# Kernel optimization log

Hardware: AMD Instinct MI355X
Metric: run time of the kernel (lower is better)

The kernel has to match this reference:

```python
import jax, jax.numpy as jnp
import numpy as np


def _conv1x1(x, W, b):
    # x: (B, Ci, H, W), W: (Co, Ci), b: (Co,)
    return jnp.einsum('oi,bihw->bohw', W, x) + b[None, :, None, None]


def setup_inputs() -> dict:
    key = jax.random.key(0)
    ks = jax.random.split(key, 12)
    B, C, H, W = 4, 256, 64, 64
    d = C // 2
    prev_c = 512
    s = lambda k, shape, scale=0.05: (jax.random.normal(k, shape, dtype=jnp.float32) * scale)
    return {
        'source_enc_f': jax.random.normal(ks[0], (B, C, H, W), dtype=jnp.float32),
        'target_enc_f': jax.random.normal(ks[1], (B, C, H, W), dtype=jnp.float32),
        'prev_inp': jax.random.normal(ks[2], (B, prev_c, H // 2, W // 2), dtype=jnp.float32),
        'Wq': s(ks[3], (d, C)), 'bq': s(ks[4], (d,)),
        'Wk': s(ks[5], (d, C)), 'bk': s(ks[6], (d,)),
        'Wv': s(ks[7], (d, C)), 'bv': s(ks[8], (d,)),
        'Wp': s(ks[9], (C, d)), 'bp': s(ks[10], (C,)),
        'gamma': jnp.zeros((1,), dtype=jnp.float32) + 0.1,  # nonzero so attn path contributes
        'Wc': s(ks[11], (C, C + prev_c, 3, 3)),
        'bc': jnp.zeros((C,), dtype=jnp.float32),
    }


def reference(source_enc_f, target_enc_f, prev_inp, Wq, bq, Wk, bk, Wv, bv, Wp, bp, gamma, Wc, bc):
    B, C, H, W = source_enc_f.shape
    d = Wq.shape[0]
    HW = H * W

    # --- AttnMech ---
    q = _conv1x1(source_enc_f, Wq, bq)   # (B, d, H, W)
    k = _conv1x1(target_enc_f, Wk, bk)
    v = _conv1x1(target_enc_f, Wv, bv)

    kf = k.reshape(B, d, HW)             # (B, d, HW)
    qf = q.reshape(B, d, HW)             # (B, d, HW)
    # scores[b, i, j] = sum_c key[b, c, i] * query[b, c, j]; no 1/sqrt(d) scaling
    scores = jnp.einsum('bci,bcj->bij', kf, qf)       # (B, HW, HW)
    attn = jax.nn.softmax(scores, axis=1)             # softmax over key axis (torch dim=1)

    vf = v.transpose(0, 2, 3, 1).reshape(B, HW, d)    # (B, HW, d)
    out = jnp.einsum('bij,bjc->bic', attn, vf)        # (B, HW, d)
    out = out.reshape(B, H, W, d).transpose(0, 3, 1, 2)  # (B, d, H, W)
    out = _conv1x1(out, Wp, bp)                       # (B, C, H, W)
    x = target_enc_f + gamma[0] * out

    # --- upsample (nearest, scale 2) + concat ---
    prev = jnp.repeat(jnp.repeat(prev_inp, 2, axis=2), 2, axis=3)
    x = jnp.concatenate([x, prev], axis=1)            # (B, C+prev_c, H, W)

    # --- 3x3 conv, stride 1, pad 1 ---
    x = jax.lax.conv_general_dilated(
        x, Wc, window_strides=(1, 1), padding=((1, 1), (1, 1)),
        dimension_numbers=('NCHW', 'OIHW', 'NCHW'))
    x = x + bc[None, :, None, None]

    # --- InstanceNorm2d (affine=False, eps=1e-5, biased var over HW) ---
    mean = jnp.mean(x, axis=(2, 3), keepdims=True)
    var = jnp.mean(jnp.square(x - mean), axis=(2, 3), keepdims=True)
    x = (x - mean) * jax.lax.rsqrt(var + 1e-5)

    return jax.nn.relu(x)
```

## Files before the change

### kernel.cpp

```cpp
#include <hip/hip_runtime.h>
#include <hip/hip_bf16.h>

#define BB 4
#define CC 256
#define HW 4096
#define DD 128

typedef __attribute__((ext_vector_type(8))) short bf16x8;
typedef __attribute__((ext_vector_type(4))) short bf16x4;
typedef __attribute__((ext_vector_type(4))) float f32x4;

static __device__ __forceinline__ void ld4(float* dst, const float* src) {
  float4 t = *(const float4*)src;
  dst[0] = t.x; dst[1] = t.y; dst[2] = t.z; dst[3] = t.w;
}

static __device__ __forceinline__ short f2b(float f) {
  unsigned u = __float_as_uint(f);
  u += 0x7fffu + ((u >> 16) & 1u);
  return (short)(u >> 16);
}
static __device__ __forceinline__ unsigned pk2(float lo, float hi) {
  return (unsigned)(unsigned short)f2b(lo) | ((unsigned)(unsigned short)f2b(hi) << 16);
}

static __device__ __forceinline__ void gl16(const short* g, short* l) {
  __builtin_amdgcn_global_load_lds(
      (const __attribute__((address_space(1))) unsigned*)g,
      (__attribute__((address_space(3))) unsigned*)l, 16, 0, 0);
}

__global__ __launch_bounds__(256) void k_qkv_mfma(
    const float* __restrict__ src, const float* __restrict__ tgt,
    const float* __restrict__ Wq, const float* __restrict__ bq,
    const float* __restrict__ Wk, const float* __restrict__ bk,
    const float* __restrict__ Wv, const float* __restrict__ bv,
    short* __restrict__ qb, short* __restrict__ kb, short* __restrict__ vb)
{
  __shared__ __align__(16) short Wt[128 * 40];
  __shared__ __align__(16) short Xt[64 * 40];
  __shared__ __align__(16) short T[9216];
  const int tid = threadIdx.x;
  const int wv = tid >> 6;
  const int lane = tid & 63;
  const int t = lane & 15, q = lane >> 4;
  const int px0 = blockIdx.x * 64;
  const int which = blockIdx.y;
  const int b = blockIdx.z;
  const float* X    = (which == 0) ? src : tgt;
  const float* Wm   = (which == 0) ? Wq : (which == 1) ? Wk : Wv;
  const float* bias = (which == 0) ? bq : (which == 1) ? bk : bv;

  const f32x4 zf = {0.f, 0.f, 0.f, 0.f};
  f32x4 acc[2][4];
#pragma unroll
  for (int mt = 0; mt < 2; ++mt)
#pragma unroll
    for (int nt = 0; nt < 4; ++nt) acc[mt][nt] = zf;

  for (int kk = 0; kk < CC; kk += 32) {
    __syncthreads();
#pragma unroll
    for (int u = 0; u < 4; ++u) {
      int e = tid + (u << 8);
      int row = e >> 3, cq = (e & 7) * 4;
      float4 w4 = *(const float4*)&Wm[row * CC + kk + cq];
      unsigned* dst = (unsigned*)(Wt + row * 40 + cq);
      dst[0] = pk2(w4.x, w4.y);
      dst[1] = pk2(w4.z, w4.w);
    }
#pragma unroll
    for (int u = 0; u < 2; ++u) {
      int e = tid + (u << 8);
      int c = e >> 4, p4 = (e & 15) * 4;
      float4 xv = *(const float4*)&X[((size_t)b * CC + kk + c) * HW + px0 + p4];
      Xt[(p4 + 0) * 40 + c] = f2b(xv.x);
      Xt[(p4 + 1) * 40 + c] = f2b(xv.y);
      Xt[(p4 + 2) * 40 + c] = f2b(xv.z);
      Xt[(p4 + 3) * 40 + c] = f2b(xv.w);
    }
    __syncthreads();
    bf16x8 af[2], bfr[4];
#pragma unroll
    for (int mt = 0; mt < 2; ++mt)
      af[mt] = *(const bf16x8*)(Wt + (wv * 32 + mt * 16 + t) * 40 + q * 8);
#pragma unroll
    for (int nt = 0; nt < 4; ++nt)
      bfr[nt] = *(const bf16x8*)(Xt + (nt * 16 + t) * 40 + q * 8);
#pragma unroll
    for (int mt = 0; mt < 2; ++mt)
#pragma unroll
      for (int nt = 0; nt < 4; ++nt)
        acc[mt][nt] = __builtin_amdgcn_mfma_f32_16x16x32_bf16(
            af[mt], bfr[nt], acc[mt][nt], 0, 0, 0);
  }
  __syncthreads();
  if (which < 2) {
#pragma unroll
    for (int mt = 0; mt < 2; ++mt) {
      int chb = wv * 32 + mt * 16 + q * 4;
#pragma unroll
      for (int r = 0; r < 4; ++r) {
        float bv_ = bias[chb + r];
#pragma unroll
        for (int nt = 0; nt < 4; ++nt)
          T[(nt * 16 + t) * 136 + chb + r] = f2b(acc[mt][nt][r] + bv_);
      }
    }
    __syncthreads();
    short* out = (which == 0) ? qb : kb;
    int p = tid >> 2, cq = (tid & 3) * 32;
    short* gdst = out + ((size_t)b * HW + px0 + p) * DD + cq;
#pragma unroll
    for (int e2 = 0; e2 < 4; ++e2)
      *(uint4*)(gdst + e2 * 8) = *(const uint4*)(T + p * 136 + cq + e2 * 8);
  } else {
#pragma unroll
    for (int mt = 0; mt < 2; ++mt) {
      int chb = wv * 32 + mt * 16 + q * 4;
#pragma unroll
      for (int r = 0; r < 4; ++r) {
        float bv_ = bias[chb + r];
#pragma unroll
        for (int nt = 0; nt < 4; ++nt)
          T[(chb + r) * 72 + nt * 16 + t] = f2b(acc[mt][nt][r] + bv_);
      }
    }
    __syncthreads();
    int ch = tid >> 1, pq = (tid & 1) * 32;
    short* gdst = vb + ((size_t)b * DD + ch) * HW + px0 + pq;
#pragma unroll
    for (int e2 = 0; e2 < 4; ++e2)
      *(uint4*)(gdst + e2 * 8) = *(const uint4*)(T + ch * 72 + pq + e2 * 8);
  }
}

__global__ __launch_bounds__(256) void k_lsum2(
    const short* __restrict__ qb, const short* __restrict__ kb,
    float* __restrict__ rl)
{
  __shared__ float lred[4][64];
  const int tid = threadIdx.x;
  const int w = tid >> 6;
  const int lane = tid & 63;
  const int t = lane & 15, q = lane >> 4;
  const int j0 = blockIdx.x * 64;
  const int ibeg = blockIdx.y * 1024;
  const int b = blockIdx.z;
  const short* qbb = qb + (size_t)b * HW * DD;
  const short* kbb = kb + (size_t)b * HW * DD;

  bf16x8 Bq[4][4];
#pragma unroll
  for (int nt = 0; nt < 4; ++nt)
#pragma unroll
    for (int kk = 0; kk < 4; ++kk)
      Bq[nt][kk] = *(const bf16x8*)(qbb + (size_t)(j0 + nt * 16 + t) * DD + kk * 32 + q * 8);

  float racc[4] = {0.f, 0.f, 0.f, 0.f};
  const f32x4 zf = {0.f, 0.f, 0.f, 0.f};

  for (int i = ibeg + w * 16; i < ibeg + 1024; i += 64) {
    bf16x8 Ak[4];
#pragma unroll
    for (int kk = 0; kk < 4; ++kk)
      Ak[kk] = *(const bf16x8*)(kbb + (size_t)(i + t) * DD + kk * 32 + q * 8);
#pragma unroll
    for (int nt = 0; nt < 4; ++nt) {
      f32x4 d = zf;
#pragma unroll
      for (int kk = 0; kk < 4; ++kk)
        d = __builtin_amdgcn_mfma_f32_16x16x32_bf16(Ak[kk], Bq[nt][kk], d, 0, 0, 0);
      racc[nt] += __expf(d[0]) + __expf(d[1]) + __expf(d[2]) + __expf(d[3]);
    }
  }
#pragma unroll
  for (int nt = 0; nt < 4; ++nt) {
    float r = racc[nt];
    r += __shfl_xor(r, 16);
    r += __shfl_xor(r, 32);
    if (q == 0) lred[w][nt * 16 + t] = r;
  }
  __syncthreads();
  if (tid < 64) {
    float sum = lred[0][tid] + lred[1][tid] + lred[2][tid] + lred[3][tid];
    atomicAdd(&rl[(size_t)b * HW + j0 + tid], sum);
  }
}

__global__ __launch_bounds__(256) void k_vs(
    const short* __restrict__ vb, const float* __restrict__ rl,
    short* __restrict__ vs)
{
  int id4 = (blockIdx.x * 256 + threadIdx.x) * 4;
  int j = id4 & (HW - 1);
  int b = id4 >> 19;
  uint2 pv = *(const uint2*)(vb + id4);
  float f0 = __uint_as_float(pv.x << 16);
  float f1 = __uint_as_float(pv.x & 0xffff0000u);
  float f2 = __uint_as_float(pv.y << 16);
  float f3 = __uint_as_float(pv.y & 0xffff0000u);
  const float* rlb = rl + (size_t)b * HW + j;
  unsigned u0 = pk2(f0 / rlb[0], f1 / rlb[1]);
  unsigned u1 = pk2(f2 / rlb[2], f3 / rlb[3]);
  *(uint2*)(vs + id4) = make_uint2(u0, u1);
}

__global__ __launch_bounds__(256, 2) void k_attn2(
    const short* __restrict__ qb, const short* __restrict__ kb,
    const short* __restrict__ vs, float* __restrict__ ao)
{
  __shared__ __align__(16) short Qs[64 * 136];
  __shared__ __align__(16) short Vss[128 * 72];
  __shared__ __align__(16) short P[4][16][76];
  const int tid = threadIdx.x;
  const int w = tid >> 6;
  const int lane = tid & 63;
  const int t = lane & 15, q = lane >> 4;
  const int b = blockIdx.z;
  const int i0 = blockIdx.x * 64 + w * 16;
  const int jbeg = blockIdx.y * 2048, jend = jbeg + 2048;
  const short* qbb = qb + (size_t)b * HW * DD;
  const short* kbb = kb + (size_t)b * HW * DD;
  const short* vsb = vs + (size_t)b * DD * HW;
  const f32x4 zf = {0.f, 0.f, 0.f, 0.f};

  bf16x8 Ak[4];
#pragma unroll
  for (int kk = 0; kk < 4; ++kk)
    Ak[kk] = *(const bf16x8*)(kbb + (size_t)(i0 + t) * DD + kk * 32 + q * 8);

  f32x4 acc[8];
#pragma unroll
  for (int nt = 0; nt < 8; ++nt) acc[nt] = zf;

  bf16x8 rq[4], rv[4];
#pragma unroll
  for (int r = 0; r < 4; ++r) {
    int e = tid + (r << 8);
    rq[r] = *(const bf16x8*)(qbb + (size_t)(jbeg + (e >> 4)) * DD + (e & 15) * 8);
    rv[r] = *(const bf16x8*)(vsb + (size_t)(e >> 3) * HW + jbeg + (e & 7) * 8);
  }

  for (int j = jbeg; j < jend; j += 64) {
    __syncthreads();
#pragma unroll
    for (int r = 0; r < 4; ++r) {
      int e = tid + (r << 8);
      *(bf16x8*)(Qs + (e >> 4) * 136 + (e & 15) * 8) = rq[r];
      *(bf16x8*)(Vss + (e >> 3) * 72 + (e & 7) * 8) = rv[r];
    }
    __syncthreads();
    if (j + 64 < jend) {
#pragma unroll
      for (int r = 0; r < 4; ++r) {
        int e = tid + (r << 8);
        rq[r] = *(const bf16x8*)(qbb + (size_t)(j + 64 + (e >> 4)) * DD + (e & 15) * 8);
        rv[r] = *(const bf16x8*)(vsb + (size_t)(e >> 3) * HW + j + 64 + (e & 7) * 8);
      }
    }
    f32x4 sv[4];
#pragma unroll
    for (int nt = 0; nt < 4; ++nt) sv[nt] = zf;
#pragma unroll
    for (int nt = 0; nt < 4; ++nt)
#pragma unroll
      for (int kk = 0; kk < 4; ++kk) {
        bf16x8 bq = *(const bf16x8*)(Qs + (nt * 16 + t) * 136 + kk * 32 + q * 8);
        sv[nt] = __builtin_amdgcn_mfma_f32_16x16x32_bf16(Ak[kk], bq, sv[nt], 0, 0, 0);
      }
#pragma unroll
    for (int nt = 0; nt < 4; ++nt)
#pragma unroll
      for (int r = 0; r < 4; ++r)
        P[w][q * 4 + r][nt * 16 + t] = f2b(__expf(sv[nt][r]));
    bf16x8 ap[2];
#pragma unroll
    for (int ks = 0; ks < 2; ++ks) {
      bf16x4 lo = *(const bf16x4*)&P[w][t][ks * 32 + q * 8];
      bf16x4 hi = *(const bf16x4*)&P[w][t][ks * 32 + q * 8 + 4];
      ap[ks] = __builtin_shufflevector(lo, hi, 0, 1, 2, 3, 4, 5, 6, 7);
    }
#pragma unroll
    for (int nt = 0; nt < 8; ++nt)
#pragma unroll
      for (int ks = 0; ks < 2; ++ks) {
        bf16x8 bv = *(const bf16x8*)(Vss + (nt * 16 + t) * 72 + ks * 32 + q * 8);
        acc[nt] = __builtin_amdgcn_mfma_f32_16x16x32_bf16(ap[ks], bv, acc[nt], 0, 0, 0);
      }
  }
  float* aob = ao + (size_t)b * DD * HW;
#pragma unroll
  for (int nt = 0; nt < 8; ++nt)
#pragma unroll
    for (int r = 0; r < 4; ++r)
      atomicAdd(&aob[(size_t)(nt * 16 + t) * HW + i0 + q * 4 + r], acc[nt][r]);
}

__global__ __launch_bounds__(256) void k_proj(
    const float* __restrict__ ao, const float* __restrict__ tgt,
    const float* __restrict__ Wp, const float* __restrict__ bp,
    const float* __restrict__ gamma, short* __restrict__ Xn)
{
  __shared__ float Wt[32][132];
  __shared__ float Xs[32][68];
  __shared__ float T[64][133];
  const int tid = threadIdx.x;
  const int tx = tid & 15, ty = tid >> 4;
  const int p0 = blockIdx.x * 64;
  const int ro = blockIdx.y * 128;
  const int b = blockIdx.z;
  const float g0 = gamma[0];

  float acc[8][4];
#pragma unroll
  for (int i = 0; i < 8; ++i)
#pragma unroll
    for (int j = 0; j < 4; ++j) acc[i][j] = 0.f;

  for (int kk = 0; kk < DD; kk += 32) {
    __syncthreads();
#pragma unroll
    for (int u = 0; u < 4; ++u) {
      int e = tid + 256 * u;
      int c4 = (e & 7) * 4, r = e >> 3;
      float w[4]; ld4(w, &Wp[(ro + r) * DD + kk + c4]);
      Wt[c4 + 0][r] = w[0]; Wt[c4 + 1][r] = w[1];
      Wt[c4 + 2][r] = w[2]; Wt[c4 + 3][r] = w[3];
    }
#pragma unroll
    for (int u = 0; u < 2; ++u) {
      int e = tid + 256 * u;
      int p4 = (e & 15) * 4, c = e >> 4;
      *(float4*)&Xs[c][p4] = *(const float4*)&ao[(b * DD + kk + c) * HW + p0 + p4];
    }
    __syncthreads();
#pragma unroll 4
    for (int c = 0; c < 32; ++c) {
      float wa[8], xb[4];
      ld4(wa, &Wt[c][ty * 8]); ld4(wa + 4, &Wt[c][ty * 8 + 4]);
      ld4(xb, &Xs[c][tx * 4]);
#pragma unroll
      for (int rr = 0; rr < 8; ++rr)
#pragma unroll
        for (int pp = 0; pp < 4; ++pp) acc[rr][pp] += wa[rr] * xb[pp];
    }
  }
#pragma unroll
  for (int rr = 0; rr < 8; ++rr) {
    int r = ro + ty * 8 + rr;
    int idx = (b * CC + r) * HW + p0 + tx * 4;
    float4 t4 = *(const float4*)&tgt[idx];
    float bpv = bp[r];
    T[tx * 4 + 0][ty * 8 + rr] = t4.x + g0 * (acc[rr][0] + bpv);
    T[tx * 4 + 1][ty * 8 + rr] = t4.y + g0 * (acc[rr][1] + bpv);
    T[tx * 4 + 2][ty * 8 + rr] = t4.z + g0 * (acc[rr][2] + bpv);
    T[tx * 4 + 3][ty * 8 + rr] = t4.w + g0 * (acc[rr][3] + bpv);
  }
  __syncthreads();
  {
    int p = tid >> 2, cq = (tid & 3) * 32;
    int h = p0 >> 6;
    unsigned* dst = (unsigned*)(Xn + ((((size_t)b * 66 + h + 1) * 66) + 1 + p) * 768 + ro + cq);
#pragma unroll
    for (int e = 0; e < 16; ++e)
      dst[e] = pk2(T[p][cq + 2 * e], T[p][cq + 2 * e + 1]);
  }
}

__global__ __launch_bounds__(256) void k_pack(
    const float* __restrict__ prev, short* __restrict__ Xn)
{
  __shared__ float tile[64][65];
  const int tid = threadIdx.x;
  const int h = blockIdx.x;
  const int ci0 = blockIdx.y * 64;
  const int b = blockIdx.z;

  {
    int w = tid & 63, r = tid >> 6;
    for (int cs = r; cs < 64; cs += 4)
      tile[cs][w] = prev[((size_t)b * 512 + ci0 + cs) * 1024 + (h >> 1) * 32 + (w >> 1)];
  }
  __syncthreads();
  {
    int ci = tid & 63, wq = tid >> 6;
    for (int ws2 = wq; ws2 < 64; ws2 += 4)
      Xn[((((size_t)b * 66 + h + 1) * 66) + 1 + ws2) * 768 + 256 + ci0 + ci] = f2b(tile[ci][ws2]);
  }
}

__global__ __launch_bounds__(256) void k_wb(
    const float* __restrict__ Wc, short* __restrict__ Wb)
{
  int i = blockIdx.x * 256 + threadIdx.x;
  int o = i / 6912;
  int rem = i - o * 6912;
  int khw = rem / 768;
  int ci = rem - khw * 768;
  Wb[i] = f2b(Wc[(size_t)o * 6912 + ci * 9 + khw]);
}

__global__ __launch_bounds__(256, 2) void k_conv_mfma(
    const short* __restrict__ Xn,
    const short* __restrict__ Wb,
    const float* __restrict__ bcw,
    short* __restrict__ cb)
{
  __shared__ __align__(16) short Wl[384 * 64];
  __shared__ __align__(16) short Xl[66 * 64];
  const int tid = threadIdx.x;
  const int wv = tid >> 6;
  const int lane = tid & 63;
  const int t = lane & 15, q = lane >> 4;
  const int h = blockIdx.x;
  const int m0blk = blockIdx.y * 128;
  const int b = blockIdx.z;

  const f32x4 zf = {0.f, 0.f, 0.f, 0.f};
  f32x4 acc[2][4];
#pragma unroll
  for (int mt = 0; mt < 2; ++mt)
#pragma unroll
    for (int nt = 0; nt < 4; ++nt) acc[mt][nt] = zf;

  for (int kh = 0; kh < 3; ++kh) {
    const short* wsrc = Wb + (size_t)m0blk * 6912 + (kh * 3) * 768;
    const short* xsrc = Xn + ((size_t)b * 66 + h + kh) * 66 * 768;
    for (int ci0 = 0; ci0 < 768; ci0 += 64) {
#pragma unroll
      for (int r = 0; r < 12; ++r) {
        int e = tid + (r << 8);
        int g = e & 7, row = e >> 3;
        int kw = row >> 7, cout = row & 127;
        int gs = g ^ (row & 7);
        gl16(wsrc + (size_t)cout * 6912 + kw * 768 + ci0 + gs * 8, Wl + e * 8);
      }
#pragma unroll
      for (int r = 0; r < 3; ++r) {
        int e = tid + (r << 8);
        if (e < 528) {
          int g = e & 7, px = e >> 3;
          int gs = g ^ (px & 7);
          gl16(xsrc + (size_t)px * 768 + ci0 + gs * 8, Xl + e * 8);
        }
      }
      __syncthreads();
#pragma unroll
      for (int kw = 0; kw < 3; ++kw) {
        bf16x8 af[2][2], bfr[4][2];
#pragma unroll
        for (int kk = 0; kk < 2; ++kk) {
#pragma unroll
          for (int mt = 0; mt < 2; ++mt) {
            int row = kw * 128 + wv * 32 + mt * 16 + t;
            int g = (kk * 4 + q) ^ (row & 7);
            af[mt][kk] = *(const bf16x8*)(Wl + row * 64 + g * 8);
          }
#pragma unroll
          for (int nt = 0; nt < 4; ++nt) {
            int row = nt * 16 + t + kw;
            int g = (kk * 4 + q) ^ (row & 7);
            bfr[nt][kk] = *(const bf16x8*)(Xl + row * 64 + g * 8);
          }
        }
#pragma unroll
        for (int kk = 0; kk < 2; ++kk)
#pragma unroll
          for (int mt = 0; mt < 2; ++mt)
#pragma unroll
            for (int nt = 0; nt < 4; ++nt)
              acc[mt][nt] = __builtin_amdgcn_mfma_f32_16x16x32_bf16(
                  af[mt][kk], bfr[nt][kk], acc[mt][nt], 0, 0, 0);
      }
      __syncthreads();
    }
  }
#pragma unroll
  for (int mt = 0; mt < 2; ++mt) {
    int om = m0blk + wv * 32 + mt * 16 + q * 4;
#pragma unroll
    for (int r = 0; r < 4; ++r) {
      float bias = bcw[om + r];
      short* orow = cb + ((size_t)b * CC + om + r) * HW + h * 64;
#pragma unroll
      for (int nt = 0; nt < 4; ++nt)
        orow[nt * 16 + t] = f2b(acc[mt][nt][r] + bias);
    }
  }
}

__global__ __launch_bounds__(256) void k_inorm(
    const short* __restrict__ cb, float* __restrict__ out)
{
  __shared__ float buf[4096];
  __shared__ float red[8];
  const int tid = threadIdx.x;
  const int ch = blockIdx.x;
  const short* srcp = cb + (size_t)ch * HW;

  float s = 0.f, sq = 0.f;
#pragma unroll
  for (int u = 0; u < 2; ++u) {
    int sidx = u * 2048 + tid * 8;
    uint4 pk = *(const uint4*)(srcp + sidx);
    float f[8];
    f[0] = __uint_as_float(pk.x << 16); f[1] = __uint_as_float(pk.x & 0xffff0000u);
    f[2] = __uint_as_float(pk.y << 16); f[3] = __uint_as_float(pk.y & 0xffff0000u);
    f[4] = __uint_as_float(pk.z << 16); f[5] = __uint_as_float(pk.z & 0xffff0000u);
    f[6] = __uint_as_float(pk.w << 16); f[7] = __uint_as_float(pk.w & 0xffff0000u);
#pragma unroll
    for (int e = 0; e < 8; ++e) {
      buf[sidx + e] = f[e];
      s += f[e];
      sq += f[e] * f[e];
    }
  }
#pragma unroll
  for (int m = 32; m >= 1; m >>= 1) {
    s  += __shfl_xor(s, m, 64);
    sq += __shfl_xor(sq, m, 64);
  }
  if ((tid & 63) == 0) { red[tid >> 6] = s; red[4 + (tid >> 6)] = sq; }
  __syncthreads();
  if (tid == 0) {
    float S = red[0] + red[1] + red[2] + red[3];
    float Q = red[4] + red[5] + red[6] + red[7];
    float mean = S * (1.f / HW);
    float var = Q * (1.f / HW) - mean * mean;
    red[0] = mean;
    red[1] = rsqrtf(var + 1e-5f);
  }
  __syncthreads();
  const float mean = red[0], rs = red[1];
#pragma unroll
  for (int u = 0; u < 4; ++u) {
    int idx = u * 1024 + tid * 4;
    float4 v = *(const float4*)&buf[idx];
    float4 o4 = make_float4(fmaxf((v.x - mean) * rs, 0.f),
                            fmaxf((v.y - mean) * rs, 0.f),
                            fmaxf((v.z - mean) * rs, 0.f),
                            fmaxf((v.w - mean) * rs, 0.f));
    *(float4*)&out[(size_t)ch * HW + idx] = o4;
  }
}

extern "C" void kernel_launch(void* const* d_in, const int* in_sizes, int n_in,
                              void* d_out, int out_size, void* d_ws, size_t ws_size,
                              hipStream_t stream) {
  const float* src  = (const float*)d_in[0];
  const float* tgt  = (const float*)d_in[1];
  const float* prev = (const float*)d_in[2];
  const float* Wq = (const float*)d_in[3];  const float* bq = (const float*)d_in[4];
  const float* Wk = (const float*)d_in[5];  const float* bk = (const float*)d_in[6];
  const float* Wv = (const float*)d_in[7];  const float* bv = (const float*)d_in[8];
  const float* Wp = (const float*)d_in[9];  const float* bp = (const float*)d_in[10];
  const float* gamma = (const float*)d_in[11];
  const float* Wc = (const float*)d_in[12]; const float* bcw = (const float*)d_in[13];

  float* ws = (float*)d_ws;
  short* qb = (short*)ws;
  short* kb = (short*)(ws + 1048576);
  short* vb = (short*)(ws + 2097152);
  float* rl = ws + 3145728;
  short* vs = (short*)(ws + 3162112);
  short* Xn = (short*)ws;
  float* ao = ws + 6690816;
  short* cb = (short*)(ws + 6690816);
  short* Wb = (short*)(ws + 8787968);

  k_qkv_mfma<<<dim3(64, 3, BB), 256, 0, stream>>>(src, tgt, Wq, bq, Wk, bk, Wv, bv, qb, kb, vb);
  hipMemsetAsync(rl, 0, (size_t)BB * HW * 4, stream);
  k_lsum2<<<dim3(64, 4, BB), 256, 0, stream>>>(qb, kb, rl);
  k_vs   <<<dim3(2048),      256, 0, stream>>>(vb, rl, vs);
  hipMemsetAsync(ao, 0, (size_t)2097152 * 4, stream);
  k_attn2<<<dim3(64, 2, BB), 256, 0, stream>>>(qb, kb, vs, ao);
  hipMemsetAsync(Xn, 0, (size_t)BB * 66 * 66 * 768 * 2, stream);
  k_proj <<<dim3(64, 2, BB), 256, 0, stream>>>(ao, tgt, Wp, bp, gamma, Xn);
  k_pack <<<dim3(64, 8, BB), 256, 0, stream>>>(prev, Xn);
  k_wb   <<<dim3(6912),      256, 0, stream>>>(Wc, Wb);
  k_conv_mfma<<<dim3(64, 2, BB), 256, 0, stream>>>(Xn, Wb, bcw, cb);
  k_inorm<<<dim3(1024),      256, 0, stream>>>(cb, (float*)d_out);
}
```

Measured before the change: 382.2 us.

## Keep attention probabilities in registers by permuting V layout in LDS

Swaps the MFMA operand order in the score product so each lane holds the transposed score tile. The exponentiated probabilities can then be packed straight into the A operand of the PV MFMA, which removes the per-wave P shared-memory round trip. To keep the k-index mapping consistent, V is stored in LDS with a permuted column order. This cuts LDS traffic, LDS capacity use and latency, at the cost of a more intricate layout whose correctness depends on the exact MFMA lane mapping.

```diff
diff --git a/kernel.cpp b/kernel.cpp
--- a/kernel.cpp
+++ b/kernel.cpp
@@ -9,6 +9,7 @@
 typedef __attribute__((ext_vector_type(8))) short bf16x8;
 typedef __attribute__((ext_vector_type(4))) short bf16x4;
 typedef __attribute__((ext_vector_type(4))) float f32x4;
+typedef __attribute__((ext_vector_type(4))) unsigned uint4v;
 
 static __device__ __forceinline__ void ld4(float* dst, const float* src) {
   float4 t = *(const float4*)src;
@@ -211,8 +212,7 @@
     const short* __restrict__ vs, float* __restrict__ ao)
 {
   __shared__ __align__(16) short Qs[64 * 136];
-  __shared__ __align__(16) short Vss[128 * 72];
-  __shared__ __align__(16) short P[4][16][76];
+  __shared__ __align__(16) short Vp[128 * 72];
   const int tid = threadIdx.x;
   const int w = tid >> 6;
   const int lane = tid & 63;
@@ -248,7 +248,16 @@
     for (int r = 0; r < 4; ++r) {
       int e = tid + (r << 8);
       *(bf16x8*)(Qs + (e >> 4) * 136 + (e & 15) * 8) = rq[r];
-      *(bf16x8*)(Vss + (e >> 3) * 72 + (e & 7) * 8) = rv[r];
+    }
+#pragma unroll
+    for (int r = 0; r < 4; ++r) {
+      int e = tid + (r << 8);
+      int c = e >> 3, u8 = e & 7;
+      int kap = (u8 >> 2) * 32 + (u8 & 1) * 16 + ((u8 >> 1) & 1) * 4;
+      bf16x4 lo = __builtin_shufflevector(rv[r], rv[r], 0, 1, 2, 3);
+      bf16x4 hi = __builtin_shufflevector(rv[r], rv[r], 4, 5, 6, 7);
+      *(bf16x4*)(Vp + c * 72 + kap) = lo;
+      *(bf16x4*)(Vp + c * 72 + kap + 8) = hi;
     }
     __syncthreads();
     if (j + 64 < jend) {
@@ -267,25 +276,23 @@
 #pragma unroll
       for (int kk = 0; kk < 4; ++kk) {
         bf16x8 bq = *(const bf16x8*)(Qs + (nt * 16 + t) * 136 + kk * 32 + q * 8);
-        sv[nt] = __builtin_amdgcn_mfma_f32_16x16x32_bf16(Ak[kk], bq, sv[nt], 0, 0, 0);
-      }
-#pragma unroll
-    for (int nt = 0; nt < 4; ++nt)
-#pragma unroll
-      for (int r = 0; r < 4; ++r)
-        P[w][q * 4 + r][nt * 16 + t] = f2b(__expf(sv[nt][r]));
+        sv[nt] = __builtin_amdgcn_mfma_f32_16x16x32_bf16(bq, Ak[kk], sv[nt], 0, 0, 0);
+      }
     bf16x8 ap[2];
 #pragma unroll
     for (int ks = 0; ks < 2; ++ks) {
-      bf16x4 lo = *(const bf16x4*)&P[w][t][ks * 32 + q * 8];
-      bf16x4 hi = *(const bf16x4*)&P[w][t][ks * 32 + q * 8 + 4];
-      ap[ks] = __builtin_shufflevector(lo, hi, 0, 1, 2, 3, 4, 5, 6, 7);
+      unsigned w0 = pk2(__expf(sv[2 * ks][0]), __expf(sv[2 * ks][1]));
+      unsigned w1 = pk2(__expf(sv[2 * ks][2]), __expf(sv[2 * ks][3]));
+      unsigned w2 = pk2(__expf(sv[2 * ks + 1][0]), __expf(sv[2 * ks + 1][1]));
+      unsigned w3 = pk2(__expf(sv[2 * ks + 1][2]), __expf(sv[2 * ks + 1][3]));
+      uint4v pw = {w0, w1, w2, w3};
+      ap[ks] = __builtin_bit_cast(bf16x8, pw);
     }
 #pragma unroll
     for (int nt = 0; nt < 8; ++nt)
 #pragma unroll
       for (int ks = 0; ks < 2; ++ks) {
-        bf16x8 bv = *(const bf16x8*)(Vss + (nt * 16 + t) * 72 + ks * 32 + q * 8);
+        bf16x8 bv = *(const bf16x8*)(Vp + (nt * 16 + t) * 72 + ks * 32 + q * 8);
         acc[nt] = __builtin_amdgcn_mfma_f32_16x16x32_bf16(ap[ks], bv, acc[nt], 0, 0, 0);
       }
   }
```

New measurement: 376.4 us. Within noise of the previous version (-1.5%).
